# Kernel tuning notes

Measured on AMD Instinct MI355X. Metric: run time of the kernel, lower is better.

Reference implementation:

```python
import jax, jax.numpy as jnp
import numpy as np

B, N, D, K, TOPK = 4, 2048, 256, 16384, 5
BASE = 1.0   # softmax base from assignment='softmax-1'
EPS = 1e-6


def setup_inputs() -> dict:
    key = jax.random.key(0)
    k1, k2, k3 = jax.random.split(key, 3)
    features = jax.random.normal(k1, (B, N, D), jnp.float32)
    attentions = jax.random.uniform(k2, (B, N, 1), jnp.float32)
    centroids = jax.random.normal(k3, (K, D), jnp.float32)
    return {"features": features, "attentions": attentions, "centroids": centroids}


def _cdist(x, c):
    # Euclidean distances [N, K] via expanded squared form (GEMM-dominant).
    x2 = jnp.sum(x * x, axis=1, keepdims=True)          # [N, 1]
    c2 = jnp.sum(c * c, axis=1)                         # [K]
    sq = x2 + c2[None, :] - 2.0 * (x @ c.T)             # [N, K]
    return jnp.sqrt(jnp.maximum(sq, 0.0))


def _assign_one(feat, att, centroids):
    # torch.cdist on detached tensors -> stop_gradient here
    d = _cdist(jax.lax.stop_gradient(feat), jax.lax.stop_gradient(centroids))  # [N, K]
    neg_top, idx = jax.lax.top_k(-d, TOPK)              # smallest distances
    dists = -neg_top                                    # [N, TOPK]
    # assignment 'softmax-1': softmax over -base*dist across the TOPK neighbors
    ass = jax.nn.softmax(-BASE * dists, axis=1)         # [N, TOPK]
    c_sel = centroids[idx]                              # [N, TOPK, D]
    # feature function 'resatt': att * (x - c)
    f = att[:, None, :] * (feat[:, None, :] - c_sel)    # [N, TOPK, D]
    desc = f * ass[..., None]                           # [N, TOPK, D]
    # scatter-add into dense per-centroid descriptor (== dense_descriptor.sum(-1))
    dense = jnp.zeros((K, D), feat.dtype).at[idx.reshape(-1)].add(desc.reshape(-1, D))
    # descriptor 'l2norm'
    grouped = dense / (jnp.linalg.norm(dense, axis=1, keepdims=True) + EPS)
    # weights 'maxass': max assignment per centroid over features (0 where unassigned)
    w = jnp.zeros((K,), feat.dtype).at[idx.reshape(-1)].max(ass.reshape(-1))
    return grouped, w


def reference(features, attentions, centroids):
    grouped, weights = jax.vmap(_assign_one, in_axes=(0, 0, None))(features, attentions, centroids)
    return grouped, weights  # [B, K, D], [B, K]
```

## Files before the change

kernel.cpp:

```cpp
#include <hip/hip_runtime.h>
#include <hip/hip_bf16.h>
#include <math.h>

#define BDIM  4
#define NFEAT 2048
#define DDIM  256
#define KCENT 16384
#define TK    5
#define NCB   4
#define CBSZ  (KCENT / NCB)
#define KB    128
#define NT    (CBSZ / KB)
#define FB    128
#define RESC  12
#define NROW  (BDIM * KCENT)
#define INFF  (__builtin_inff())

typedef __attribute__((ext_vector_type(4))) float  f32x4;
typedef __attribute__((ext_vector_type(8))) short  short8v;

static __device__ __forceinline__ short f2bf(float x) {
  __hip_bfloat16 h = __float2bfloat16(x);
  return __builtin_bit_cast(short, h);
}

static __device__ __forceinline__ float wsum(float v) {
  v += __shfl_xor(v, 1);  v += __shfl_xor(v, 2);  v += __shfl_xor(v, 4);
  v += __shfl_xor(v, 8);  v += __shfl_xor(v, 16); v += __shfl_xor(v, 32);
  return v;
}
static __device__ __forceinline__ unsigned uwsum(unsigned v) {
  v += __shfl_xor(v, 1);  v += __shfl_xor(v, 2);  v += __shfl_xor(v, 4);
  v += __shfl_xor(v, 8);  v += __shfl_xor(v, 16); v += __shfl_xor(v, 32);
  return v;
}
static __device__ __forceinline__ unsigned med3u(unsigned a, unsigned b, unsigned c) {
  unsigned d;
  asm("v_med3_u32 %0, %1, %2, %3" : "=v"(d) : "v"(a), "v"(b), "v"(c));
  return d;
}

__global__ __launch_bounds__(256) void k_cvtall(const float* __restrict__ F,
                                                const float* __restrict__ C,
                                                short* __restrict__ Xbf,
                                                short* __restrict__ Cbf,
                                                float* __restrict__ c2) {
  if (blockIdx.x < 1024) {
    const int i = blockIdx.x * 256 + threadIdx.x;
    const float4* s = (const float4*)F + (size_t)i * 2;
    const float4 a = s[0], b = s[1];
    short8v o;
    o[0] = f2bf(a.x); o[1] = f2bf(a.y); o[2] = f2bf(a.z); o[3] = f2bf(a.w);
    o[4] = f2bf(b.x); o[5] = f2bf(b.y); o[6] = f2bf(b.z); o[7] = f2bf(b.w);
    ((short8v*)Xbf)[i] = o;
  } else {
    const int w = threadIdx.x >> 6, l = threadIdx.x & 63;
    const int row = (blockIdx.x - 1024) * 4 + w;
    const float4 v = *(const float4*)(C + (size_t)row * DDIM + l * 4);
    short4 o;
    o.x = f2bf(v.x); o.y = f2bf(v.y); o.z = f2bf(v.z); o.w = f2bf(v.w);
    *(short4*)(Cbf + (size_t)row * DDIM + l * 4) = o;
    const float ss = wsum(v.x*v.x + v.y*v.y + v.z*v.z + v.w*v.w);
    if (l == 0) c2[row] = ss;
  }
}

__global__ __launch_bounds__(1024, 4) void k_main(
    const short* __restrict__ Xbf, const short* __restrict__ Cbf,
    const float* __restrict__ c2g, uint2* __restrict__ cand)
{
  __shared__ short sC[2][KB * DDIM];
  __shared__ float sC2a[CBSZ];

  const int tid = threadIdx.x;
  const int l = tid & 63, w = tid >> 6;
  const int wm = w & 3, wn = w >> 2;
  const int lrow = l & 15, lk = l >> 4;
  const int cb = blockIdx.x & (NCB - 1), fb = blockIdx.x / NCB;
  const int fbase = fb * FB;
  const size_t coffB = (size_t)cb * CBSZ * (DDIM * 2);

  const int poff = (tid >> 9) * 8192 + (tid & 15) * 512 +
                   ((tid >> 6) & 7) * 64 + ((tid >> 4) & 3) * 16;

  auto stage = [&](const char* gsrcB, int buf) {
#pragma unroll
    for (int r = 0; r < 4; ++r) {
      __builtin_amdgcn_global_load_lds(
          (const __attribute__((address_space(1))) void*)(gsrcB + r * 16384 + poff),
          (__attribute__((address_space(3))) void*)((char*)&sC[buf][0] + r * 16384 + tid * 16),
          16, 0, 0);
    }
  };

  stage((const char*)Xbf + (size_t)fbase * 512, 1);
  stage((const char*)Cbf + coffB, 0);
  {
    const f32x4* src = (const f32x4*)(c2g + cb * CBSZ);
    const f32x4 bias = {1024.f, 1024.f, 1024.f, 1024.f};
    ((f32x4*)sC2a)[tid] = src[tid] + bias;
  }
  __syncthreads();

  short8v bfr[2][8];
#pragma unroll
  for (int nf = 0; nf < 2; ++nf) {
    const char* bp = (const char*)&sC[1][0] + (wn * 2 + nf) * 8192 + l * 16;
#pragma unroll
    for (int kk = 0; kk < 8; ++kk)
      bfr[nf][kk] = *(const short8v*)(bp + kk * 1024);
  }
  __syncthreads();

  const char* a0b0 = (const char*)&sC[0][0] + (wm * 2 + 0) * 8192 + l * 16;
  const char* a1b0 = (const char*)&sC[0][0] + (wm * 2 + 1) * 8192 + l * 16;
  const char* a0b1 = (const char*)&sC[1][0] + (wm * 2 + 0) * 8192 + l * 16;
  const char* a1b1 = (const char*)&sC[1][0] + (wm * 2 + 1) * 8192 + l * 16;

  unsigned kv[2][5];
#pragma unroll
  for (int nf = 0; nf < 2; ++nf)
#pragma unroll
    for (int j = 0; j < 5; ++j) kv[nf][j] = 0xFFFFFFFFu;

  for (int t = 0; t < NT; ++t) {
    const int buf = t & 1;
    if (t + 1 < NT) {
      stage((const char*)Cbf + coffB + (size_t)(t + 1) * (KB * 512), buf ^ 1);
      __builtin_amdgcn_sched_barrier(0);
      asm volatile("s_waitcnt vmcnt(4)" ::: "memory");
    } else {
      __builtin_amdgcn_sched_barrier(0);
      asm volatile("s_waitcnt vmcnt(0)" ::: "memory");
    }
    __builtin_amdgcn_s_barrier();
    __builtin_amdgcn_sched_barrier(0);

    f32x4 acc[2][2];
    const f32x4 z = {0.f, 0.f, 0.f, 0.f};
#pragma unroll
    for (int mf = 0; mf < 2; ++mf)
#pragma unroll
      for (int nf = 0; nf < 2; ++nf) acc[mf][nf] = z;

    const char* ap0 = buf ? a0b1 : a0b0;
    const char* ap1 = buf ? a1b1 : a1b0;
#pragma unroll
    for (int kk = 0; kk < 8; ++kk) {
      const short8v a0 = *(const short8v*)(ap0 + kk * 1024);
      const short8v a1 = *(const short8v*)(ap1 + kk * 1024);
#pragma unroll
      for (int nf = 0; nf < 2; ++nf) {
        acc[0][nf] = __builtin_amdgcn_mfma_f32_16x16x32_bf16(a0, bfr[nf][kk], acc[0][nf], 0, 0, 0);
        acc[1][nf] = __builtin_amdgcn_mfma_f32_16x16x32_bf16(a1, bfr[nf][kk], acc[1][nf], 0, 0, 0);
      }
    }

    const f32x4 cb0 = *(const f32x4*)&sC2a[t * KB + wm * 32 + lk * 4];
    const f32x4 cb1 = *(const f32x4*)&sC2a[t * KB + wm * 32 + 16 + lk * 4];
#pragma unroll
    for (int mf = 0; mf < 2; ++mf)
#pragma unroll
      for (int r = 0; r < 4; ++r) {
        const float c2v = mf ? cb1[r] : cb0[r];
        const unsigned q = (unsigned)(t * 8 + mf * 4 + r);
#pragma unroll
        for (int nf = 0; nf < 2; ++nf) {
          const float sqb = fmaf(-2.0f, acc[mf][nf][r], c2v);
          const unsigned x = (__float_as_uint(sqb) & 0xFFFFFF00u) | q;
          const unsigned a0 = kv[nf][0], a1 = kv[nf][1], a2 = kv[nf][2],
                         a3 = kv[nf][3], a4 = kv[nf][4];
          kv[nf][0] = a0 < x ? a0 : x;
          kv[nf][1] = med3u(a0, a1, x);
          kv[nf][2] = med3u(a1, a2, x);
          kv[nf][3] = med3u(a2, a3, x);
          kv[nf][4] = med3u(a3, a4, x);
        }
      }

    __builtin_amdgcn_sched_barrier(0);
    asm volatile("s_waitcnt lgkmcnt(0)" ::: "memory");
    __builtin_amdgcn_s_barrier();
    __builtin_amdgcn_sched_barrier(0);
  }

  unsigned* mb = (unsigned*)&sC[0][0];
#pragma unroll
  for (int nf = 0; nf < 2; ++nf) {
    const int fl = wn * 32 + nf * 16 + lrow;
    const int s = wm * 4 + lk;
#pragma unroll
    for (int j = 0; j < 5; ++j) mb[fl * 81 + s * 5 + j] = kv[nf][j];
  }
  __syncthreads();

  if (tid < FB) {
    unsigned bv[8], bi[8];
#pragma unroll
    for (int j = 0; j < 8; ++j) { bv[j] = 0xFFFFFFFFu; bi[j] = 0; }
    const unsigned* row = mb + tid * 81;
    for (int s = 0; s < 16; ++s) {
      const unsigned aux = (unsigned)(cb * CBSZ + (s >> 2) * 32 + (s & 3) * 4);
#pragma unroll
      for (int j = 0; j < 5; ++j) {
        const unsigned v = row[s * 5 + j];
        const unsigned q = v & 255u;
        const unsigned ci = aux + (q >> 3) * 128 + ((q >> 2) & 1u) * 16 + (q & 3u);
        const bool s0 = v < bv[0], s1 = v < bv[1], s2 = v < bv[2], s3 = v < bv[3],
                   s4 = v < bv[4], s5 = v < bv[5], s6 = v < bv[6], s7 = v < bv[7];
        bv[7] = s6 ? bv[6] : (s7 ? v : bv[7]);  bi[7] = s6 ? bi[6] : (s7 ? ci : bi[7]);
        bv[6] = s5 ? bv[5] : (s6 ? v : bv[6]);  bi[6] = s5 ? bi[5] : (s6 ? ci : bi[6]);
        bv[5] = s4 ? bv[4] : (s5 ? v : bv[5]);  bi[5] = s4 ? bi[4] : (s5 ? ci : bi[5]);
        bv[4] = s3 ? bv[3] : (s4 ? v : bv[4]);  bi[4] = s3 ? bi[3] : (s4 ? ci : bi[4]);
        bv[3] = s2 ? bv[2] : (s3 ? v : bv[3]);  bi[3] = s2 ? bi[2] : (s3 ? ci : bi[3]);
        bv[2] = s1 ? bv[1] : (s2 ? v : bv[2]);  bi[2] = s1 ? bi[1] : (s2 ? ci : bi[2]);
        bv[1] = s0 ? bv[0] : (s1 ? v : bv[1]);  bi[1] = s0 ? bi[0] : (s1 ? ci : bi[1]);
        bv[0] = s0 ? v : bv[0];                 bi[0] = s0 ? ci : bi[0];
      }
    }
    uint2* cp = cand + ((size_t)(fbase + tid) * NCB + cb) * 8;
#pragma unroll
    for (int j = 0; j < 8; ++j) cp[j] = make_uint2(bv[j], bi[j]);
  }
}

__global__ __launch_bounds__(256) void k_select(
    const float* __restrict__ F, const float* __restrict__ A,
    const float* __restrict__ C, const float* __restrict__ c2g,
    const uint2* __restrict__ cand, uint4* __restrict__ sel,
    unsigned* __restrict__ cnt)
{
  const int l = threadIdx.x & 63, w = threadIdx.x >> 6;
  const int f = blockIdx.x * 4 + w;
  const int b = f >> 11;

  const float4 xv = *(const float4*)(F + (size_t)f * DDIM + l * 4);
  const float x2 = wsum(xv.x*xv.x + xv.y*xv.y + xv.z*xv.z + xv.w*xv.w);

  unsigned key = 0xFFFFFFFFu, ci = 0u;
  if (l < 32) { const uint2 e = cand[(size_t)f * 32 + l]; key = e.x; ci = e.y; }

#pragma unroll
  for (int k = 2; k <= 32; k <<= 1) {
#pragma unroll
    for (int j = k >> 1; j >= 1; j >>= 1) {
      const unsigned pk = __shfl_xor(key, j);
      const unsigned pc = __shfl_xor(ci, j);
      const bool keepMin = (((l & j) == 0) == ((l & k) == 0));
      const bool take = keepMin ? (pk < key) : (pk > key);
      if (take) { key = pk; ci = pc; }
    }
  }

  int sidx[RESC];
#pragma unroll
  for (int j = 0; j < RESC; ++j) sidx[j] = __shfl((int)ci, j);
  float4 cv[RESC];
#pragma unroll
  for (int j = 0; j < RESC; ++j)
    cv[j] = *(const float4*)(C + (size_t)sidx[j] * DDIM + l * 4);
  float sq[RESC];
#pragma unroll
  for (int j = 0; j < RESC; ++j) {
    const float d = wsum(xv.x*cv[j].x + xv.y*cv[j].y + xv.z*cv[j].z + xv.w*cv[j].w);
    sq[j] = fmaxf(fmaf(-2.0f, d, x2 + c2g[sidx[j]]), 0.0f);
  }

  unsigned sk[RESC];
#pragma unroll
  for (int j = 0; j < RESC; ++j) sk[j] = (__float_as_uint(sq[j]) & ~15u) | (unsigned)j;
  float ssq[TK]; int jm5[TK];
#pragma unroll
  for (int s = 0; s < TK; ++s) {
    unsigned m = 0xFFFFFFFFu;
#pragma unroll
    for (int j = 0; j < RESC; ++j) m = sk[j] < m ? sk[j] : m;
#pragma unroll
    for (int j = 0; j < RESC; ++j) sk[j] = (sk[j] == m) ? 0xFFFFFFFFu : sk[j];
    ssq[s] = __uint_as_float(m & ~15u);
    jm5[s] = (int)(m & 15u);
  }
  int k5[TK];
#pragma unroll
  for (int s = 0; s < TK; ++s) k5[s] = __shfl((int)ci, jm5[s]);

  const float d0 = sqrtf(ssq[0]);
  float p5[TK]; float sum = 0.f;
#pragma unroll
  for (int s = 0; s < TK; ++s) { p5[s] = expf(d0 - sqrtf(ssq[s])); sum += p5[s]; }
  const float inv = 1.0f / sum;
  const float att = A[f];

  float p = p5[0]; int ks = k5[0];
  p = (l == 1) ? p5[1] : p;  ks = (l == 1) ? k5[1] : ks;
  p = (l == 2) ? p5[2] : p;  ks = (l == 2) ? k5[2] : ks;
  p = (l == 3) ? p5[3] : p;  ks = (l == 3) ? k5[3] : ks;
  p = (l == 4) ? p5[4] : p;  ks = (l == 4) ? k5[4] : ks;
  p *= inv;
  if (l < TK) {
    sel[(size_t)f * TK + l] = make_uint4((unsigned)ks, __float_as_uint(p),
                                         __float_as_uint(att * p), 0u);
    atomicAdd(&cnt[b * KCENT + ks], 1u);
  }
}

__global__ __launch_bounds__(256) void k_scan1(const unsigned* __restrict__ cnt,
                                               unsigned* __restrict__ bsum) {
  __shared__ unsigned ws4[4];
  const int t = threadIdx.x, lane = t & 63, w = t >> 6;
  const uint4 c = *(const uint4*)&cnt[(blockIdx.x * 256 + t) * 4];
  unsigned v = uwsum(c.x + c.y + c.z + c.w);
  if (lane == 0) ws4[w] = v;
  __syncthreads();
  if (t == 0) bsum[blockIdx.x] = ws4[0] + ws4[1] + ws4[2] + ws4[3];
}

__global__ __launch_bounds__(64) void k_scan2(const unsigned* __restrict__ bsum,
                                              unsigned* __restrict__ boff) {
  const int l = threadIdx.x;
  unsigned v = bsum[l];
  const unsigned own = v;
#pragma unroll
  for (int d = 1; d < 64; d <<= 1) {
    const unsigned n = __shfl_up(v, d);
    if (l >= d) v += n;
  }
  boff[l] = v - own;
}

__global__ __launch_bounds__(256) void k_scan3(const unsigned* __restrict__ cnt,
                                               const unsigned* __restrict__ boff,
                                               unsigned* __restrict__ off) {
  __shared__ unsigned wt[4];
  const int t = threadIdx.x, lane = t & 63, w = t >> 6;
  const int i0 = (blockIdx.x * 256 + t) * 4;
  const uint4 c = *(const uint4*)&cnt[i0];
  const unsigned ts = c.x + c.y + c.z + c.w;
  unsigned v = ts;
#pragma unroll
  for (int d = 1; d < 64; d <<= 1) {
    const unsigned n = __shfl_up(v, d);
    if (lane >= d) v += n;
  }
  if (lane == 63) wt[w] = v;
  __syncthreads();
  unsigned wb = boff[blockIdx.x];
  if (w > 0) wb += wt[0];
  if (w > 1) wb += wt[1];
  if (w > 2) wb += wt[2];
  const unsigned ex = wb + v - ts;
  uint4 o;
  o.x = ex; o.y = ex + c.x; o.z = o.y + c.y; o.w = o.z + c.z;
  *(uint4*)&off[i0] = o;
}

__global__ __launch_bounds__(256) void k_fill(const uint4* __restrict__ sel,
                                              unsigned* __restrict__ off,
                                              uint4* __restrict__ ent) {
  const int f = blockIdx.x * 256 + threadIdx.x;
  const int b = f >> 11;
#pragma unroll
  for (int s = 0; s < TK; ++s) {
    const uint4 e = sel[(size_t)f * TK + s];
    const unsigned pos = atomicAdd(&off[b * KCENT + (int)e.x], 1u);
    ent[pos] = make_uint4((unsigned)f, e.y, e.z, 0u);
  }
}

__global__ __launch_bounds__(256) void k_out(
    const float* __restrict__ F, const float* __restrict__ C,
    const unsigned* __restrict__ cnt, const unsigned* __restrict__ offend,
    const uint4* __restrict__ ent, float* __restrict__ outG, float* __restrict__ outW)
{
  const int l = threadIdx.x & 63, w = threadIdx.x >> 6;
  const int row = blockIdx.x * 4 + w;
  const int k = row & (KCENT - 1);
  const unsigned c = cnt[row];
  const unsigned s0 = offend[row] - c;

  float4 acc = {0.f, 0.f, 0.f, 0.f};
  float csum = 0.f, pmax = 0.f;
  for (unsigned j = 0; j < c; ++j) {
    const uint4 E = ent[s0 + j];
    const float coef = __uint_as_float(E.z);
    const float pp = __uint_as_float(E.y);
    const float4 xr = *(const float4*)(F + (size_t)E.x * DDIM + l * 4);
    acc.x = fmaf(coef, xr.x, acc.x);
    acc.y = fmaf(coef, xr.y, acc.y);
    acc.z = fmaf(coef, xr.z, acc.z);
    acc.w = fmaf(coef, xr.w, acc.w);
    csum += coef; pmax = fmaxf(pmax, pp);
  }
  float4 o = {0.f, 0.f, 0.f, 0.f};
  if (c > 0) {
    const float4 cv = *(const float4*)(C + (size_t)k * DDIM + l * 4);
    o.x = fmaf(-csum, cv.x, acc.x);
    o.y = fmaf(-csum, cv.y, acc.y);
    o.z = fmaf(-csum, cv.z, acc.z);
    o.w = fmaf(-csum, cv.w, acc.w);
    const float ss = wsum(o.x*o.x + o.y*o.y + o.z*o.z + o.w*o.w);
    const float sc = 1.0f / (sqrtf(ss) + 1e-6f);
    o.x *= sc; o.y *= sc; o.z *= sc; o.w *= sc;
  }
  *(float4*)(outG + (size_t)row * DDIM + l * 4) = o;
  if (l == 0) outW[row] = pmax;
}

extern "C" void kernel_launch(void* const* d_in, const int* in_sizes, int n_in,
                              void* d_out, int out_size, void* d_ws, size_t ws_size,
                              hipStream_t stream) {
  const float* F = (const float*)d_in[0];
  const float* A = (const float*)d_in[1];
  const float* C = (const float*)d_in[2];
  float* outG = (float*)d_out;
  float* outW = outG + (size_t)BDIM * KCENT * DDIM;

  char* ws = (char*)d_ws;
  short*    Xbf  = (short*)ws;
  short*    Cbf  = (short*)(ws + (4u << 20));
  float*    c2   = (float*)(ws + (12u << 20));
  uint2*    cand = (uint2*)(ws + (13u << 20));
  uint4*    sel  = (uint4*)ws;
  unsigned* cnt  = (unsigned*)(ws + (1u << 20));
  unsigned* off  = (unsigned*)(ws + (1536u << 10));
  unsigned* bsum = (unsigned*)(ws + (1792u << 10));
  unsigned* boff = (unsigned*)(ws + (1796u << 10));
  uint4*    ent  = (uint4*)(ws + (2u << 20));

  k_cvtall<<<1024 + KCENT / 4, 256, 0, stream>>>(F, C, Xbf, Cbf, c2);
  k_main  <<<(BDIM * NFEAT / FB) * NCB, 1024, 0, stream>>>(Xbf, Cbf, c2, cand);
  hipMemsetAsync(cnt, 0, NROW * sizeof(unsigned), stream);
  k_select<<<BDIM * NFEAT / 4, 256, 0, stream>>>(F, A, C, c2, cand, sel, cnt);
  k_scan1 <<<NROW / 1024, 256, 0, stream>>>(cnt, bsum);
  k_scan2 <<<1, 64, 0, stream>>>(bsum, boff);
  k_scan3 <<<NROW / 1024, 256, 0, stream>>>(cnt, boff, off);
  k_fill  <<<BDIM * NFEAT / 256, 256, 0, stream>>>(sel, off, ent);
  k_out   <<<NROW / 4, 256, 0, stream>>>(F, C, cnt, off, ent, outG, outW);
}
```

Before: 187.8 us.

## Fold count zeroing into convert kernel, merge scans, remap main block order

The separate memset of the per-centroid counts moves into extra blocks of the conversion kernel, and the three-kernel prefix scan becomes one single-block 1024-thread scan. The aim is to cut launch count and per-launch overhead on small kernels. The main GEMM kernel's block-to-(centroid block, feature block) mapping is also reordered so adjacent blocks share centroid tiles, which may improve L2 reuse. The cost is that the single-block scan runs serially on one CU over 65536 counters. The counts buffer also moves into the workspace region after c2.

Result: slower. 199.5 us (+6.2%).

```diff
diff --git a/kernel.cpp b/kernel.cpp
--- a/kernel.cpp
+++ b/kernel.cpp
@@ -29,11 +29,6 @@
   v += __shfl_xor(v, 8);  v += __shfl_xor(v, 16); v += __shfl_xor(v, 32);
   return v;
 }
-static __device__ __forceinline__ unsigned uwsum(unsigned v) {
-  v += __shfl_xor(v, 1);  v += __shfl_xor(v, 2);  v += __shfl_xor(v, 4);
-  v += __shfl_xor(v, 8);  v += __shfl_xor(v, 16); v += __shfl_xor(v, 32);
-  return v;
-}
 static __device__ __forceinline__ unsigned med3u(unsigned a, unsigned b, unsigned c) {
   unsigned d;
   asm("v_med3_u32 %0, %1, %2, %3" : "=v"(d) : "v"(a), "v"(b), "v"(c));
@@ -44,7 +39,8 @@
                                                 const float* __restrict__ C,
                                                 short* __restrict__ Xbf,
                                                 short* __restrict__ Cbf,
-                                                float* __restrict__ c2) {
+                                                float* __restrict__ c2,
+                                                unsigned* __restrict__ cnt) {
   if (blockIdx.x < 1024) {
     const int i = blockIdx.x * 256 + threadIdx.x;
     const float4* s = (const float4*)F + (size_t)i * 2;
@@ -53,7 +49,7 @@
     o[0] = f2bf(a.x); o[1] = f2bf(a.y); o[2] = f2bf(a.z); o[3] = f2bf(a.w);
     o[4] = f2bf(b.x); o[5] = f2bf(b.y); o[6] = f2bf(b.z); o[7] = f2bf(b.w);
     ((short8v*)Xbf)[i] = o;
-  } else {
+  } else if (blockIdx.x < 1024 + KCENT / 4) {
     const int w = threadIdx.x >> 6, l = threadIdx.x & 63;
     const int row = (blockIdx.x - 1024) * 4 + w;
     const float4 v = *(const float4*)(C + (size_t)row * DDIM + l * 4);
@@ -62,6 +58,9 @@
     *(short4*)(Cbf + (size_t)row * DDIM + l * 4) = o;
     const float ss = wsum(v.x*v.x + v.y*v.y + v.z*v.z + v.w*v.w);
     if (l == 0) c2[row] = ss;
+  } else {
+    const int i = (blockIdx.x - (1024 + KCENT / 4)) * 256 + threadIdx.x;
+    ((uint4*)cnt)[i] = make_uint4(0u, 0u, 0u, 0u);
   }
 }
 
@@ -76,7 +75,8 @@
   const int l = tid & 63, w = tid >> 6;
   const int wm = w & 3, wn = w >> 2;
   const int lrow = l & 15, lk = l >> 4;
-  const int cb = blockIdx.x & (NCB - 1), fb = blockIdx.x / NCB;
+  const int cb = (blockIdx.x & 7) >> 1;
+  const int fb = (blockIdx.x >> 3) * 2 + (blockIdx.x & 1);
   const int fbase = fb * FB;
   const size_t coffB = (size_t)cb * CBSZ * (DDIM * 2);
 
@@ -304,54 +304,38 @@
   }
 }
 
-__global__ __launch_bounds__(256) void k_scan1(const unsigned* __restrict__ cnt,
-                                               unsigned* __restrict__ bsum) {
-  __shared__ unsigned ws4[4];
+__global__ __launch_bounds__(1024) void k_scan(const unsigned* __restrict__ cnt,
+                                               unsigned* __restrict__ off) {
+  __shared__ unsigned wt[16];
   const int t = threadIdx.x, lane = t & 63, w = t >> 6;
-  const uint4 c = *(const uint4*)&cnt[(blockIdx.x * 256 + t) * 4];
-  unsigned v = uwsum(c.x + c.y + c.z + c.w);
-  if (lane == 0) ws4[w] = v;
+  const uint4* src = (const uint4*)cnt + t * 16;
+  uint4 v[16];
+  unsigned tot = 0;
+#pragma unroll
+  for (int i = 0; i < 16; ++i) {
+    v[i] = src[i];
+    tot += v[i].x + v[i].y + v[i].z + v[i].w;
+  }
+  unsigned ws = tot;
+#pragma unroll
+  for (int d = 1; d < 64; d <<= 1) {
+    const unsigned n = __shfl_up(ws, d);
+    if (lane >= d) ws += n;
+  }
+  if (lane == 63) wt[w] = ws;
   __syncthreads();
-  if (t == 0) bsum[blockIdx.x] = ws4[0] + ws4[1] + ws4[2] + ws4[3];
-}
-
-__global__ __launch_bounds__(64) void k_scan2(const unsigned* __restrict__ bsum,
-                                              unsigned* __restrict__ boff) {
-  const int l = threadIdx.x;
-  unsigned v = bsum[l];
-  const unsigned own = v;
-#pragma unroll
-  for (int d = 1; d < 64; d <<= 1) {
-    const unsigned n = __shfl_up(v, d);
-    if (l >= d) v += n;
-  }
-  boff[l] = v - own;
-}
-
-__global__ __launch_bounds__(256) void k_scan3(const unsigned* __restrict__ cnt,
-                                               const unsigned* __restrict__ boff,
-                                               unsigned* __restrict__ off) {
-  __shared__ unsigned wt[4];
-  const int t = threadIdx.x, lane = t & 63, w = t >> 6;
-  const int i0 = (blockIdx.x * 256 + t) * 4;
-  const uint4 c = *(const uint4*)&cnt[i0];
-  const unsigned ts = c.x + c.y + c.z + c.w;
-  unsigned v = ts;
-#pragma unroll
-  for (int d = 1; d < 64; d <<= 1) {
-    const unsigned n = __shfl_up(v, d);
-    if (lane >= d) v += n;
-  }
-  if (lane == 63) wt[w] = v;
-  __syncthreads();
-  unsigned wb = boff[blockIdx.x];
-  if (w > 0) wb += wt[0];
-  if (w > 1) wb += wt[1];
-  if (w > 2) wb += wt[2];
-  const unsigned ex = wb + v - ts;
-  uint4 o;
-  o.x = ex; o.y = ex + c.x; o.z = o.y + c.y; o.w = o.z + c.z;
-  *(uint4*)&off[i0] = o;
+  unsigned wbase = 0;
+#pragma unroll
+  for (int j = 0; j < 16; ++j) wbase += (j < w) ? wt[j] : 0u;
+  unsigned ex = wbase + ws - tot;
+  uint4* dst = (uint4*)off + t * 16;
+#pragma unroll
+  for (int i = 0; i < 16; ++i) {
+    uint4 o;
+    o.x = ex; o.y = ex + v[i].x; o.z = o.y + v[i].y; o.w = o.z + v[i].z;
+    ex = o.w + v[i].w;
+    dst[i] = o;
+  }
 }
 
 __global__ __launch_bounds__(256) void k_fill(const uint4* __restrict__ sel,
@@ -419,21 +403,16 @@
   short*    Xbf  = (short*)ws;
   short*    Cbf  = (short*)(ws + (4u << 20));
   float*    c2   = (float*)(ws + (12u << 20));
+  unsigned* cnt  = (unsigned*)(ws + (12u << 20) + (64u << 10));
   uint2*    cand = (uint2*)(ws + (13u << 20));
   uint4*    sel  = (uint4*)ws;
-  unsigned* cnt  = (unsigned*)(ws + (1u << 20));
   unsigned* off  = (unsigned*)(ws + (1536u << 10));
-  unsigned* bsum = (unsigned*)(ws + (1792u << 10));
-  unsigned* boff = (unsigned*)(ws + (1796u << 10));
   uint4*    ent  = (uint4*)(ws + (2u << 20));
 
-  k_cvtall<<<1024 + KCENT / 4, 256, 0, stream>>>(F, C, Xbf, Cbf, c2);
+  k_cvtall<<<1024 + KCENT / 4 + 64, 256, 0, stream>>>(F, C, Xbf, Cbf, c2, cnt);
   k_main  <<<(BDIM * NFEAT / FB) * NCB, 1024, 0, stream>>>(Xbf, Cbf, c2, cand);
-  hipMemsetAsync(cnt, 0, NROW * sizeof(unsigned), stream);
   k_select<<<BDIM * NFEAT / 4, 256, 0, stream>>>(F, A, C, c2, cand, sel, cnt);
-  k_scan1 <<<NROW / 1024, 256, 0, stream>>>(cnt, bsum);
-  k_scan2 <<<1, 64, 0, stream>>>(bsum, boff);
-  k_scan3 <<<NROW / 1024, 256, 0, stream>>>(cnt, boff, off);
+  k_scan  <<<1, 1024, 0, stream>>>(cnt, off);
   k_fill  <<<BDIM * NFEAT / 256, 256, 0, stream>>>(sel, off, ent);
   k_out   <<<NROW / 4, 256, 0, stream>>>(F, C, cnt, off, ent, outG, outW);
 }
```
